# Kernel tuning notes

Hardware: AMD Instinct MI355X
Metric: run time of the kernel (lower is better)

The kernel has to match this reference:

```python
import jax, jax.numpy as jnp
import numpy as np

D, NH, NL, NP, NLAYERS, DFF = 256, 8, 4, 4, 6, 1024
DH = D // NH
SHAPES = [(96, 96), (48, 48), (24, 24), (12, 12)]
STARTS = np.concatenate([[0], np.cumsum([h * w for h, w in SHAPES])[:-1]]).tolist()
LQ = sum(h * w for h, w in SHAPES)
B = 2


def setup_inputs():
    ks = iter(jax.random.split(jax.random.key(0), 64))
    inp = {}
    for i, (h, w) in enumerate(SHAPES):
        inp[f"src{i}"] = jax.random.normal(next(ks), (B, D, h, w), jnp.float32)
        inp[f"pos{i}"] = jax.random.normal(next(ks), (B, D, h, w), jnp.float32) * 0.1
    inp["level_embed"] = jax.random.normal(next(ks), (NL, D), jnp.float32) * 0.02
    W = lambda s, sc: jax.random.normal(next(ks), s, jnp.float32) * sc
    inp["W_off"] = W((NLAYERS, D, NH * NL * NP * 2), 0.01)
    inp["b_off"] = W((NLAYERS, NH * NL * NP * 2), 0.5)
    inp["W_attn"] = W((NLAYERS, D, NH * NL * NP), 0.02)
    inp["b_attn"] = W((NLAYERS, NH * NL * NP), 0.02)
    inp["W_val"] = W((NLAYERS, D, D), 0.05)
    inp["b_val"] = jnp.zeros((NLAYERS, D), jnp.float32)
    inp["W_out"] = W((NLAYERS, D, D), 0.05)
    inp["b_out"] = jnp.zeros((NLAYERS, D), jnp.float32)
    inp["ln1_g"] = jnp.ones((NLAYERS, D), jnp.float32)
    inp["ln1_b"] = jnp.zeros((NLAYERS, D), jnp.float32)
    inp["W_ffn1"] = W((NLAYERS, D, DFF), 0.05)
    inp["b_ffn1"] = jnp.zeros((NLAYERS, DFF), jnp.float32)
    inp["W_ffn2"] = W((NLAYERS, DFF, D), 0.05)
    inp["b_ffn2"] = jnp.zeros((NLAYERS, D), jnp.float32)
    inp["ln2_g"] = jnp.ones((NLAYERS, D), jnp.float32)
    inp["ln2_b"] = jnp.zeros((NLAYERS, D), jnp.float32)
    return inp


def layer_norm(x, g, b):
    mu = x.mean(-1, keepdims=True)
    var = ((x - mu) ** 2).mean(-1, keepdims=True)
    return (x - mu) * jax.lax.rsqrt(var + 1e-5) * g + b


def reference_points():
    refs = []
    for h, w in SHAPES:
        ys = (jnp.arange(h, dtype=jnp.float32) + 0.5) / h
        xs = (jnp.arange(w, dtype=jnp.float32) + 0.5) / w
        gy, gx = jnp.meshgrid(ys, xs, indexing="ij")
        refs.append(jnp.stack([gx.reshape(-1), gy.reshape(-1)], -1))
    return jnp.concatenate(refs, 0)  # [LQ, 2] (x, y); valid_ratios==1 so level-independent


def bilinear(v, loc, H_, W_):
    # v: [B, H*W, NH, DH]; loc: [B, LQ, NH, NP, 2] normalized to [0,1]
    # matches F.grid_sample(mode='bilinear', padding_mode='zeros', align_corners=False)
    x = loc[..., 0] * W_ - 0.5
    y = loc[..., 1] * H_ - 0.5
    x0f, y0f = jnp.floor(x), jnp.floor(y)
    lx, ly = x - x0f, y - y0f
    x0, y0 = x0f.astype(jnp.int32), y0f.astype(jnp.int32)

    def g(xi, yi):
        valid = ((xi >= 0) & (xi < W_) & (yi >= 0) & (yi < H_)).astype(v.dtype)
        flat = jnp.clip(yi, 0, H_ - 1) * W_ + jnp.clip(xi, 0, W_ - 1)  # [B,LQ,NH,NP]
        idx = flat.transpose(0, 1, 3, 2).reshape(B, LQ * NP, NH)
        got = jnp.take_along_axis(v, jnp.broadcast_to(idx[..., None], (B, LQ * NP, NH, DH)), axis=1)
        got = got.reshape(B, LQ, NP, NH, DH).transpose(0, 1, 3, 2, 4)  # [B,LQ,NH,NP,DH]
        return got * valid[..., None]

    return (g(x0, y0) * ((1 - lx) * (1 - ly))[..., None]
            + g(x0 + 1, y0) * (lx * (1 - ly))[..., None]
            + g(x0, y0 + 1) * ((1 - lx) * ly)[..., None]
            + g(x0 + 1, y0 + 1) * (lx * ly)[..., None])


def reference(src0, src1, src2, src3, pos0, pos1, pos2, pos3, level_embed,
              W_off, b_off, W_attn, b_attn, W_val, b_val, W_out, b_out,
              ln1_g, ln1_b, W_ffn1, b_ffn1, W_ffn2, b_ffn2, ln2_g, ln2_b):
    srcs = [src0, src1, src2, src3]
    poss = [pos0, pos1, pos2, pos3]
    x = jnp.concatenate([s.reshape(B, D, -1).transpose(0, 2, 1) for s in srcs], 1)  # [B,LQ,D]
    pos = jnp.concatenate(
        [p.reshape(B, D, -1).transpose(0, 2, 1) + level_embed[i][None, None] for i, p in enumerate(poss)], 1)
    ref = reference_points()  # [LQ,2]
    norm = jnp.array([[w, h] for h, w in SHAPES], jnp.float32)  # [NL,2] = (W,H)

    for li in range(NLAYERS):
        q = x + pos
        off = (q @ W_off[li] + b_off[li]).reshape(B, LQ, NH, NL, NP, 2)
        attn = jax.nn.softmax((q @ W_attn[li] + b_attn[li]).reshape(B, LQ, NH, NL * NP), -1)
        attn = attn.reshape(B, LQ, NH, NL, NP)
        val = (x @ W_val[li] + b_val[li]).reshape(B, LQ, NH, DH)
        loc = ref[None, :, None, None, None, :] + off / norm[None, None, None, :, None, :]
        out = jnp.zeros((B, LQ, NH, DH), x.dtype)
        for l, (h, w) in enumerate(SHAPES):
            vl = val[:, STARTS[l]:STARTS[l] + h * w]
            sampled = bilinear(vl, loc[:, :, :, l], h, w)  # [B,LQ,NH,NP,DH]
            out = out + (sampled * attn[:, :, :, l, :, None]).sum(3)
        out = out.reshape(B, LQ, D) @ W_out[li] + b_out[li]
        x = layer_norm(x + out, ln1_g[li], ln1_b[li])
        ffn = jax.nn.relu(x @ W_ffn1[li] + b_ffn1[li]) @ W_ffn2[li] + b_ffn2[li]
        x = layer_norm(x + ffn, ln2_g[li], ln2_b[li])
    return x
```

## Files before the change

### kernel.cpp

```cpp
#include <hip/hip_runtime.h>
#include <stdint.h>

#define NHEAD  8
#define NLAYER 6
#define BATCH  2
#define LQ     12240
#define MTOK   (BATCH*LQ)
#define MPAD   24576

typedef __attribute__((ext_vector_type(8))) short bf16x8;
typedef __attribute__((ext_vector_type(4))) float f32x4;
typedef __attribute__((ext_vector_type(4))) short s16x4;

__device__ __forceinline__ unsigned short f2bf(float f) {
  union { float f; uint32_t u; } v; v.f = f;
  uint32_t u = v.u;
  uint32_t r = (u + 0x7fffu + ((u >> 16) & 1u)) >> 16;
  return (unsigned short)r;
}
__device__ __forceinline__ float bf2f(unsigned short s) {
  union { uint32_t u; float f; } v; v.u = ((uint32_t)s) << 16;
  return v.f;
}
__device__ __forceinline__ float hi_bf(uint32_t u) {
  union { uint32_t u; float f; } v; v.u = u & 0xffff0000u; return v.f;
}
__device__ __forceinline__ float lo_bf(uint32_t u) {
  union { uint32_t u; float f; } v; v.u = u << 16; return v.f;
}

template<int EPI, int BM>
__global__ __launch_bounds__(256)
void gemm_kernel(const unsigned short* __restrict__ A,
                 const unsigned short* __restrict__ BT,
                 const float* __restrict__ bias,
                 float* __restrict__ Cf,
                 unsigned short* __restrict__ Cb,
                 int K, int ldc)
{
  constexpr int MT = BM / 32;
  __shared__ unsigned short lA[BM*64];
  __shared__ unsigned short lB[128*64];
  const int tid  = threadIdx.x;
  const int lane = tid & 63;
  const int wm = ((tid >> 6) >> 1) * (BM/2);
  const int wn = ((tid >> 6) & 1) * 64;
  const size_t row0 = (size_t)blockIdx.x * BM;
  const size_t col0 = (size_t)blockIdx.y * 128;

  f32x4 acc[MT][4] = {};

  for (int kt = 0; kt < K; kt += 64) {
#pragma unroll
    for (int i = 0; i < MT; ++i) {
      const int slot = i*256 + tid;
      const int r  = slot >> 3;
      const int cs = (slot & 7) ^ (r & 7);
      const unsigned short* ga = A + (row0 + r) * (size_t)K + kt + cs*8;
      __builtin_amdgcn_global_load_lds(
          (const __attribute__((address_space(1))) uint32_t*)ga,
          (__attribute__((address_space(3))) uint32_t*)(&lA[slot*8]), 16, 0, 0);
    }
#pragma unroll
    for (int i = 0; i < 4; ++i) {
      const int slot = i*256 + tid;
      const int r  = slot >> 3;
      const int cs = (slot & 7) ^ (r & 7);
      const unsigned short* gb = BT + (col0 + r) * (size_t)K + kt + cs*8;
      __builtin_amdgcn_global_load_lds(
          (const __attribute__((address_space(1))) uint32_t*)gb,
          (__attribute__((address_space(3))) uint32_t*)(&lB[slot*8]), 16, 0, 0);
    }
    __syncthreads();
#pragma unroll
    for (int kk = 0; kk < 2; ++kk) {
      bf16x8 af[MT], bfv[4];
#pragma unroll
      for (int m = 0; m < MT; ++m) {
        const int r  = wm + m*16 + (lane & 15);
        const int ch = (kk*4 + (lane >> 4)) ^ (r & 7);
        af[m] = *(const bf16x8*)(&lA[r*64 + ch*8]);
      }
#pragma unroll
      for (int n = 0; n < 4; ++n) {
        const int r  = wn + n*16 + (lane & 15);
        const int ch = (kk*4 + (lane >> 4)) ^ (r & 7);
        bfv[n] = *(const bf16x8*)(&lB[r*64 + ch*8]);
      }
#pragma unroll
      for (int m = 0; m < MT; ++m)
#pragma unroll
        for (int n = 0; n < 4; ++n)
          acc[m][n] = __builtin_amdgcn_mfma_f32_16x16x32_bf16(af[m], bfv[n], acc[m][n], 0, 0, 0);
    }
    __syncthreads();
  }

  const int lq = lane >> 4;
  const int lr = lane & 15;
#pragma unroll
  for (int n = 0; n < 4; ++n) {
    const int col = (int)col0 + wn + n*16 + lr;
    const float bv = bias ? bias[col] : 0.f;
#pragma unroll
    for (int m = 0; m < MT; ++m) {
      const size_t rb = row0 + wm + m*16 + lq*4;
#pragma unroll
      for (int i = 0; i < 4; ++i) {
        float v = acc[m][n][i] + bv;
        if (EPI == 2) v = fmaxf(v, 0.f);
        if (EPI == 0) Cf[(rb + i) * (size_t)ldc + col] = v;
        else          Cb[(rb + i) * (size_t)ldc + col] = f2bf(v);
      }
    }
  }
}

template<int MODE>
__global__ __launch_bounds__(256)
void gemm_ln_kernel(const unsigned short* __restrict__ A,
                    const unsigned short* __restrict__ BT,
                    const float* __restrict__ bias,
                    const float* __restrict__ xres,
                    const float* __restrict__ g,
                    const float* __restrict__ bn,
                    const float* __restrict__ posf,
                    float* __restrict__ xoutf,
                    unsigned short* __restrict__ xbf,
                    unsigned short* __restrict__ qbf,
                    float* __restrict__ dout,
                    int K)
{
  __shared__ unsigned short lA[32*64];
  __shared__ unsigned short lB[256*64];
  __shared__ float rs1[4][32];
  __shared__ float rs2[4][32];
  const int tid  = threadIdx.x;
  const int lane = tid & 63;
  const int w    = tid >> 6;
  const size_t row0 = (size_t)blockIdx.x * 32;

  f32x4 acc[2][4] = {};

  for (int kt = 0; kt < K; kt += 64) {
    {
      const int slot = tid;
      const int r  = slot >> 3;
      const int cs = (slot & 7) ^ (r & 7);
      const unsigned short* ga = A + (row0 + r) * (size_t)K + kt + cs*8;
      __builtin_amdgcn_global_load_lds(
          (const __attribute__((address_space(1))) uint32_t*)ga,
          (__attribute__((address_space(3))) uint32_t*)(&lA[slot*8]), 16, 0, 0);
    }
#pragma unroll
    for (int i = 0; i < 8; ++i) {
      const int slot = i*256 + tid;
      const int r  = slot >> 3;
      const int cs = (slot & 7) ^ (r & 7);
      const unsigned short* gb = BT + (size_t)r * K + kt + cs*8;
      __builtin_amdgcn_global_load_lds(
          (const __attribute__((address_space(1))) uint32_t*)gb,
          (__attribute__((address_space(3))) uint32_t*)(&lB[slot*8]), 16, 0, 0);
    }
    __syncthreads();
#pragma unroll
    for (int kk = 0; kk < 2; ++kk) {
      bf16x8 af[2], bfv[4];
#pragma unroll
      for (int m = 0; m < 2; ++m) {
        const int r  = m*16 + (lane & 15);
        const int ch = (kk*4 + (lane >> 4)) ^ (r & 7);
        af[m] = *(const bf16x8*)(&lA[r*64 + ch*8]);
      }
#pragma unroll
      for (int n = 0; n < 4; ++n) {
        const int r  = w*64 + n*16 + (lane & 15);
        const int ch = (kk*4 + (lane >> 4)) ^ (r & 7);
        bfv[n] = *(const bf16x8*)(&lB[r*64 + ch*8]);
      }
#pragma unroll
      for (int m = 0; m < 2; ++m)
#pragma unroll
        for (int n = 0; n < 4; ++n)
          acc[m][n] = __builtin_amdgcn_mfma_f32_16x16x32_bf16(af[m], bfv[n], acc[m][n], 0, 0, 0);
    }
    __syncthreads();
  }

  const int lq = lane >> 4;
  const int lr = lane & 15;
  float bcol[4], gcol[4], bncol[4];
#pragma unroll
  for (int n = 0; n < 4; ++n) {
    const int c = w*64 + n*16 + lr;
    bcol[n]  = bias[c];
    gcol[n]  = g[c];
    bncol[n] = bn[c];
  }
#pragma unroll
  for (int m = 0; m < 2; ++m)
#pragma unroll
    for (int i = 0; i < 4; ++i) {
      const size_t row = row0 + m*16 + lq*4 + i;
#pragma unroll
      for (int n = 0; n < 4; ++n)
        acc[m][n][i] += bcol[n] + xres[row*256 + w*64 + n*16 + lr];
    }
#pragma unroll
  for (int m = 0; m < 2; ++m)
#pragma unroll
    for (int i = 0; i < 4; ++i) {
      float t1 = acc[m][0][i] + acc[m][1][i] + acc[m][2][i] + acc[m][3][i];
      float t2 = acc[m][0][i]*acc[m][0][i] + acc[m][1][i]*acc[m][1][i]
               + acc[m][2][i]*acc[m][2][i] + acc[m][3][i]*acc[m][3][i];
#pragma unroll
      for (int o = 1; o < 16; o <<= 1) {
        t1 += __shfl_xor(t1, o, 64);
        t2 += __shfl_xor(t2, o, 64);
      }
      if (lr == 0) {
        rs1[w][m*16 + lq*4 + i] = t1;
        rs2[w][m*16 + lq*4 + i] = t2;
      }
    }
  __syncthreads();
#pragma unroll
  for (int m = 0; m < 2; ++m)
#pragma unroll
    for (int i = 0; i < 4; ++i) {
      const int r = m*16 + lq*4 + i;
      const float s1 = rs1[0][r] + rs1[1][r] + rs1[2][r] + rs1[3][r];
      const float s2 = rs2[0][r] + rs2[1][r] + rs2[2][r] + rs2[3][r];
      const float mu  = s1 * (1.f/256.f);
      const float var = s2 * (1.f/256.f) - mu*mu;
      const float rstd = rsqrtf(var + 1e-5f);
      const size_t row = row0 + r;
#pragma unroll
      for (int n = 0; n < 4; ++n) {
        const int c = w*64 + n*16 + lr;
        const float nv = (acc[m][n][i] - mu) * rstd * gcol[n] + bncol[n];
        const size_t idx = row*256 + c;
        if (MODE == 2) {
          if (row < MTOK) dout[idx] = nv;
        } else {
          xoutf[idx] = nv;
          xbf[idx]   = f2bf(nv);
          if (MODE == 1) qbf[idx] = f2bf(nv + posf[idx]);
        }
      }
    }
}

__global__ void pack_kernel(const float* __restrict__ s0, const float* __restrict__ s1,
                            const float* __restrict__ s2, const float* __restrict__ s3,
                            const float* __restrict__ p0, const float* __restrict__ p1,
                            const float* __restrict__ p2, const float* __restrict__ p3,
                            const float* __restrict__ lev,
                            float* __restrict__ xo, float* __restrict__ po)
{
  const int bt = blockIdx.x;
  int lvl, st;
  if      (bt < 288) { lvl = 0; st = bt; }
  else if (bt < 360) { lvl = 1; st = bt - 288; }
  else if (bt < 378) { lvl = 2; st = bt - 360; }
  else               { lvl = 3; st = bt - 378; }
  const int HWs[4] = {9216, 2304, 576, 144};
  const int LSs[4] = {0, 9216, 11520, 12096};
  const int hw = HWs[lvl], ls = LSs[lvl];
  const int b = blockIdx.z & 1, isp = blockIdx.z >> 1;
  const float* ins[8] = {s0, s1, s2, s3, p0, p1, p2, p3};
  const float* in = ins[isp*4 + lvl];
  const int sbase = st*32, d0 = blockIdx.y*32;
  __shared__ float tile[32][33];
  const int tx = threadIdx.x, ty = threadIdx.y;
#pragma unroll
  for (int j = 0; j < 4; ++j) {
    int ss = sbase + tx;
    int dd = d0 + ty + j*8;
    tile[ty + j*8][tx] = (ss < hw) ? in[((size_t)b*256 + dd)*hw + ss] : 0.f;
  }
  __syncthreads();
  const float addv = isp ? lev[lvl*256 + d0 + tx] : 0.f;
  float* outp = isp ? po : xo;
#pragma unroll
  for (int j = 0; j < 4; ++j) {
    int ss = sbase + ty + j*8;
    if (ss < hw)
      outp[(size_t)(b*LQ + ls + ss)*256 + d0 + tx] = tile[tx][ty + j*8] + addv;
  }
}

__global__ void wtrans_kernel(const float* __restrict__ Woff, const float* __restrict__ Watt,
                              const float* __restrict__ Wval, const float* __restrict__ Wout,
                              const float* __restrict__ Wf1,  const float* __restrict__ Wf2,
                              unsigned short* __restrict__ WoaT, unsigned short* __restrict__ WvalT,
                              unsigned short* __restrict__ WoutT, unsigned short* __restrict__ Wf1T,
                              unsigned short* __restrict__ Wf2T)
{
  const int li = blockIdx.z;
  const int bt = blockIdx.x;
  const float* in; unsigned short* out; int Kd, Nd, tn, tIdx;
  if      (bt < 64)  { in = Woff + (size_t)li*65536;  out = WoaT  + (size_t)li*98304;         Kd=256;  Nd=256;  tn=8;  tIdx=bt; }
  else if (bt < 96)  { in = Watt + (size_t)li*32768;  out = WoaT  + (size_t)li*98304 + 65536; Kd=256;  Nd=128;  tn=4;  tIdx=bt-64; }
  else if (bt < 160) { in = Wval + (size_t)li*65536;  out = WvalT + (size_t)li*65536;         Kd=256;  Nd=256;  tn=8;  tIdx=bt-96; }
  else if (bt < 224) { in = Wout + (size_t)li*65536;  out = WoutT + (size_t)li*65536;         Kd=256;  Nd=256;  tn=8;  tIdx=bt-160; }
  else if (bt < 480) { in = Wf1  + (size_t)li*262144; out = Wf1T  + (size_t)li*262144;        Kd=256;  Nd=1024; tn=32; tIdx=bt-224; }
  else               { in = Wf2  + (size_t)li*262144; out = Wf2T  + (size_t)li*262144;        Kd=1024; Nd=256;  tn=8;  tIdx=bt-480; }
  const int kt = tIdx / tn, nt = tIdx - kt*tn;
  const int k0 = kt*32, n0 = nt*32;
  __shared__ float tile[32][33];
  const int tx = threadIdx.x, ty = threadIdx.y;
#pragma unroll
  for (int j = 0; j < 4; ++j)
    tile[ty + j*8][tx] = in[(size_t)(k0 + ty + j*8) * Nd + n0 + tx];
  __syncthreads();
#pragma unroll
  for (int j = 0; j < 4; ++j)
    out[(size_t)(n0 + ty + j*8) * Kd + k0 + tx] = f2bf(tile[tx][ty + j*8]);
}

__global__ void bias_concat_kernel(const float* __restrict__ boff, const float* __restrict__ batt,
                                   float* __restrict__ boa)
{
  const int li = blockIdx.x, i = threadIdx.x;
  boa[li*384 + i] = (i < 256) ? boff[li*256 + i] : batt[li*128 + (i - 256)];
}

__global__ void prep_kernel(const float* __restrict__ x, const float* __restrict__ pos,
                            unsigned short* __restrict__ xbf, unsigned short* __restrict__ qbf)
{
  const int idx = blockIdx.x * 256 + threadIdx.x;
  const int row = idx >> 6;
  s16x4 xb = {}, qb = {};
  if (row < MTOK) {
    const f32x4 xv = *(const f32x4*)(x + (size_t)idx*4);
    const f32x4 pv = *(const f32x4*)(pos + (size_t)idx*4);
#pragma unroll
    for (int j = 0; j < 4; ++j) {
      xb[j] = (short)f2bf(xv[j]);
      qb[j] = (short)f2bf(xv[j] + pv[j]);
    }
  }
  *(s16x4*)(xbf + (size_t)idx*4) = xb;
  *(s16x4*)(qbf + (size_t)idx*4) = qb;
}

__global__ __launch_bounds__(256)
void sample_kernel(const float* __restrict__ Coa, const unsigned short* __restrict__ val,
                   unsigned short* __restrict__ outbf)
{
  __shared__ int4  pdo[32][17];
  __shared__ f32x4 pdw[32][17];
  const int tid = threadIdx.x;
  const int gi  = tid >> 3;
  const int g   = blockIdx.x * 32 + gi;
  const int t   = g >> 3, h = g & 7;
  const int b   = (t >= LQ) ? 1 : 0;

  {
    const int i0 = tid & 7;
    int4  ov0 = {0,0,0,0}, ov1 = {0,0,0,0};
    f32x4 wv0 = {0,0,0,0}, wv1 = {0,0,0,0};
    if (t < MTOK) {
      const int q = t - b * LQ;
      float refx, refy;
      if      (q < 9216)  { const int r = q;         const int rw = r/96; refx = (r - rw*96 + 0.5f)*(1.f/96.f); refy = (rw + 0.5f)*(1.f/96.f); }
      else if (q < 11520) { const int r = q - 9216;  const int rw = r/48; refx = (r - rw*48 + 0.5f)*(1.f/48.f); refy = (rw + 0.5f)*(1.f/48.f); }
      else if (q < 12096) { const int r = q - 11520; const int rw = r/24; refx = (r - rw*24 + 0.5f)*(1.f/24.f); refy = (rw + 0.5f)*(1.f/24.f); }
      else                { const int r = q - 12096; const int rw = r/12; refx = (r - rw*12 + 0.5f)*(1.f/12.f); refy = (rw + 0.5f)*(1.f/12.f); }
      const size_t crow = (size_t)t * 384;
      const float l0 = Coa[crow + 256 + h*16 + i0];
      const float l1 = Coa[crow + 256 + h*16 + i0 + 8];
      float mx = fmaxf(l0, l1);
#pragma unroll
      for (int m = 1; m < 8; m <<= 1) mx = fmaxf(mx, __shfl_xor(mx, m, 64));
      const float e0 = __expf(l0 - mx), e1 = __expf(l1 - mx);
      float sum = e0 + e1;
#pragma unroll
      for (int m = 1; m < 8; m <<= 1) sum += __shfl_xor(sum, m, 64);
      const float inv = 1.f / sum;

      auto mkpd = [&](int i, float aw, int4& ov, f32x4& wv) {
        const int l    = i >> 2;
        const int wl   = (l == 0) ? 96 : (l == 1) ? 48 : (l == 2) ? 24 : 12;
        const int base = (l == 0) ? 0  : (l == 1) ? 9216 : (l == 2) ? 11520 : 12096;
        const float ox = Coa[crow + h*32 + 2*i];
        const float oy = Coa[crow + h*32 + 2*i + 1];
        const float fw = (float)wl;
        const float xx = refx*fw + ox - 0.5f;
        const float yy = refy*fw + oy - 0.5f;
        const float xf = floorf(xx), yf = floorf(yy);
        const int x0 = (int)xf, y0 = (int)yf;
        const float lx = xx - xf, ly = yy - yf;
        const bool vx0 = (x0   >= 0) & (x0   < wl);
        const bool vx1 = (x0+1 >= 0) & (x0+1 < wl);
        const bool vy0 = (y0   >= 0) & (y0   < wl);
        const bool vy1 = (y0+1 >= 0) & (y0+1 < wl);
        const int cx0 = min(max(x0,   0), wl-1);
        const int cx1 = min(max(x0+1, 0), wl-1);
        const int cy0 = min(max(y0,   0), wl-1);
        const int cy1 = min(max(y0+1, 0), wl-1);
        ov.x = (base + cy0*wl + cx0) * 512;
        ov.y = (base + cy0*wl + cx1) * 512;
        ov.z = (base + cy1*wl + cx0) * 512;
        ov.w = (base + cy1*wl + cx1) * 512;
        wv[0] = (vx0 & vy0) ? (1.f-lx)*(1.f-ly)*aw : 0.f;
        wv[1] = (vx1 & vy0) ? lx*(1.f-ly)*aw       : 0.f;
        wv[2] = (vx0 & vy1) ? (1.f-lx)*ly*aw       : 0.f;
        wv[3] = (vx1 & vy1) ? lx*ly*aw             : 0.f;
      };
      mkpd(i0,     e0 * inv, ov0, wv0);
      mkpd(i0 + 8, e1 * inv, ov1, wv1);
    }
    pdo[gi][i0]     = ov0;  pdw[gi][i0]     = wv0;
    pdo[gi][i0 + 8] = ov1;  pdw[gi][i0 + 8] = wv1;
  }
  __syncthreads();

  const int lane8 = tid & 7;
  const char* vb = (const char*)(val + (size_t)b*LQ*256 + h*32 + lane8*4);
  const int4*  po8 = pdo[gi];
  const f32x4* pw8 = pdw[gi];
  f32x4 a0 = {}, a1 = {}, a2 = {}, a3 = {};
#pragma unroll
  for (int p = 0; p < 16; ++p) {
    const int4  o = po8[p];
    const f32x4 w = pw8[p];
    const uint2 c0 = *(const uint2*)(vb + o.x);
    const uint2 c1 = *(const uint2*)(vb + o.y);
    const uint2 c2 = *(const uint2*)(vb + o.z);
    const uint2 c3 = *(const uint2*)(vb + o.w);
    a0[0] += w[0]*lo_bf(c0.x); a0[1] += w[0]*hi_bf(c0.x); a0[2] += w[0]*lo_bf(c0.y); a0[3] += w[0]*hi_bf(c0.y);
    a1[0] += w[1]*lo_bf(c1.x); a1[1] += w[1]*hi_bf(c1.x); a1[2] += w[1]*lo_bf(c1.y); a1[3] += w[1]*hi_bf(c1.y);
    a2[0] += w[2]*lo_bf(c2.x); a2[1] += w[2]*hi_bf(c2.x); a2[2] += w[2]*lo_bf(c2.y); a2[3] += w[2]*hi_bf(c2.y);
    a3[0] += w[3]*lo_bf(c3.x); a3[1] += w[3]*hi_bf(c3.x); a3[2] += w[3]*lo_bf(c3.y); a3[3] += w[3]*hi_bf(c3.y);
  }
  s16x4 ob;
#pragma unroll
  for (int j = 0; j < 4; ++j) ob[j] = (short)f2bf((a0[j] + a1[j]) + (a2[j] + a3[j]));
  *(s16x4*)(outbf + (size_t)t*256 + h*32 + lane8*4) = ob;
}

extern "C" void kernel_launch(void* const* d_in, const int* in_sizes, int n_in,
                              void* d_out, int out_size, void* d_ws, size_t ws_size,
                              hipStream_t stream)
{
  const float* src0 = (const float*)d_in[0];
  const float* pos0 = (const float*)d_in[1];
  const float* src1 = (const float*)d_in[2];
  const float* pos1 = (const float*)d_in[3];
  const float* src2 = (const float*)d_in[4];
  const float* pos2 = (const float*)d_in[5];
  const float* src3 = (const float*)d_in[6];
  const float* pos3 = (const float*)d_in[7];
  const float* lev  = (const float*)d_in[8];
  const float* W_off= (const float*)d_in[9];
  const float* b_off= (const float*)d_in[10];
  const float* W_att= (const float*)d_in[11];
  const float* b_att= (const float*)d_in[12];
  const float* W_val= (const float*)d_in[13];
  const float* b_val= (const float*)d_in[14];
  const float* W_out= (const float*)d_in[15];
  const float* b_out= (const float*)d_in[16];
  const float* ln1g = (const float*)d_in[17];
  const float* ln1b = (const float*)d_in[18];
  const float* W_f1 = (const float*)d_in[19];
  const float* b_f1 = (const float*)d_in[20];
  const float* W_f2 = (const float*)d_in[21];
  const float* b_f2 = (const float*)d_in[22];
  const float* ln2g = (const float*)d_in[23];
  const float* ln2b = (const float*)d_in[24];

  char* wp = (char*)d_ws;
  auto take = [&](size_t bytes) { char* p = wp; wp += (bytes + 255) & ~(size_t)255; return p; };
  float* x    = (float*)take((size_t)MPAD*256*4);
  float* pos  = (float*)take((size_t)MPAD*256*4);
  float* Coa  = (float*)take((size_t)MPAD*384*4);
  unsigned short* xbf    = (unsigned short*)take((size_t)MPAD*256*2);
  unsigned short* qbf    = (unsigned short*)take((size_t)MPAD*256*2);
  unsigned short* valbf  = (unsigned short*)take((size_t)MPAD*256*2);
  unsigned short* sampbf = (unsigned short*)take((size_t)MPAD*256*2);
  unsigned short* h1bf   = (unsigned short*)take((size_t)MPAD*1024*2);
  unsigned short* WoaT   = (unsigned short*)take((size_t)NLAYER*384*256*2);
  unsigned short* WvalT  = (unsigned short*)take((size_t)NLAYER*256*256*2);
  unsigned short* WoutT  = (unsigned short*)take((size_t)NLAYER*256*256*2);
  unsigned short* Wf1T   = (unsigned short*)take((size_t)NLAYER*1024*256*2);
  unsigned short* Wf2T   = (unsigned short*)take((size_t)NLAYER*256*1024*2);
  float* boa  = (float*)take((size_t)NLAYER*384*4);

  dim3 tb(32, 8);
  pack_kernel<<<dim3(383, 8, 4), tb, 0, stream>>>(src0, src1, src2, src3,
                                                  pos0, pos1, pos2, pos3, lev, x, pos);
  wtrans_kernel<<<dim3(736, 1, 6), tb, 0, stream>>>(W_off, W_att, W_val, W_out, W_f1, W_f2,
                                                    WoaT, WvalT, WoutT, Wf1T, Wf2T);
  bias_concat_kernel<<<NLAYER, 384, 0, stream>>>(b_off, b_att, boa);
  prep_kernel<<<MPAD/4, 256, 0, stream>>>(x, pos, xbf, qbf);

  for (int li = 0; li < NLAYER; ++li) {
    gemm_kernel<0,64><<<dim3(MPAD/64, 3), 256, 0, stream>>>(qbf, WoaT + (size_t)li*98304,
        boa + li*384, Coa, nullptr, 256, 384);
    gemm_kernel<1,64><<<dim3(MPAD/64, 2), 256, 0, stream>>>(xbf, WvalT + (size_t)li*65536,
        b_val + li*256, nullptr, valbf, 256, 256);
    sample_kernel<<<MPAD/4, 256, 0, stream>>>(Coa, valbf, sampbf);
    gemm_ln_kernel<0><<<MPAD/32, 256, 0, stream>>>(sampbf, WoutT + (size_t)li*65536,
        b_out + li*256, x, ln1g + li*256, ln1b + li*256, nullptr,
        x, xbf, nullptr, nullptr, 256);
    gemm_kernel<2,128><<<dim3(MPAD/128, 8), 256, 0, stream>>>(xbf, Wf1T + (size_t)li*262144,
        b_f1 + li*1024, nullptr, h1bf, 256, 1024);
    if (li < NLAYER-1)
      gemm_ln_kernel<1><<<MPAD/32, 256, 0, stream>>>(h1bf, Wf2T + (size_t)li*262144,
          b_f2 + li*256, x, ln2g + li*256, ln2b + li*256, pos,
          x, xbf, qbf, nullptr, 1024);
    else
      gemm_ln_kernel<2><<<MPAD/32, 256, 0, stream>>>(h1bf, Wf2T + (size_t)li*262144,
          b_f2 + li*256, x, ln2g + li*256, ln2b + li*256, nullptr,
          nullptr, nullptr, nullptr, (float*)d_out, 1024);
  }
}
```

Measured before the change: 996.2 us.

## Store value head-major and gather adjacent bilinear corners with one contiguous load

```diff
diff --git a/kernel.cpp b/kernel.cpp
--- a/kernel.cpp
+++ b/kernel.cpp
@@ -109,8 +109,19 @@
       for (int i = 0; i < 4; ++i) {
         float v = acc[m][n][i] + bv;
         if (EPI == 2) v = fmaxf(v, 0.f);
-        if (EPI == 0) Cf[(rb + i) * (size_t)ldc + col] = v;
-        else          Cb[(rb + i) * (size_t)ldc + col] = f2bf(v);
+        if (EPI == 3) {
+          const size_t row = rb + i;
+          if (row < MTOK) {
+            const int bb = (row >= LQ) ? 1 : 0;
+            const int q  = (int)row - bb * LQ;
+            const int hh = col >> 5, ch = col & 31;
+            Cb[((size_t)(bb*8 + hh) * LQ + q) * 32 + ch] = f2bf(v);
+          }
+        } else if (EPI == 0) {
+          Cf[(rb + i) * (size_t)ldc + col] = v;
+        } else {
+          Cb[(rb + i) * (size_t)ldc + col] = f2bf(v);
+        }
       }
     }
   }
@@ -346,21 +357,21 @@
 }
 
 __global__ __launch_bounds__(256)
-void sample_kernel(const float* __restrict__ Coa, const unsigned short* __restrict__ val,
+void sample_kernel(const float* __restrict__ Coa, const unsigned short* __restrict__ valh,
                    unsigned short* __restrict__ outbf)
 {
-  __shared__ int4  pdo[32][17];
-  __shared__ f32x4 pdw[32][17];
+  __shared__ int2  pdo[16][16];
+  __shared__ f32x4 pdw[16][16];
   const int tid = threadIdx.x;
-  const int gi  = tid >> 3;
-  const int g   = blockIdx.x * 32 + gi;
+  const int gi  = tid >> 4;
+  const int g   = blockIdx.x * 16 + gi;
   const int t   = g >> 3, h = g & 7;
   const int b   = (t >= LQ) ? 1 : 0;
 
   {
-    const int i0 = tid & 7;
-    int4  ov0 = {0,0,0,0}, ov1 = {0,0,0,0};
-    f32x4 wv0 = {0,0,0,0}, wv1 = {0,0,0,0};
+    const int i = tid & 15;
+    int2  ov = {0, 0};
+    f32x4 wv = {0.f, 0.f, 0.f, 0.f};
     if (t < MTOK) {
       const int q = t - b * LQ;
       float refx, refy;
@@ -369,76 +380,77 @@
       else if (q < 12096) { const int r = q - 11520; const int rw = r/24; refx = (r - rw*24 + 0.5f)*(1.f/24.f); refy = (rw + 0.5f)*(1.f/24.f); }
       else                { const int r = q - 12096; const int rw = r/12; refx = (r - rw*12 + 0.5f)*(1.f/12.f); refy = (rw + 0.5f)*(1.f/12.f); }
       const size_t crow = (size_t)t * 384;
-      const float l0 = Coa[crow + 256 + h*16 + i0];
-      const float l1 = Coa[crow + 256 + h*16 + i0 + 8];
-      float mx = fmaxf(l0, l1);
-#pragma unroll
-      for (int m = 1; m < 8; m <<= 1) mx = fmaxf(mx, __shfl_xor(mx, m, 64));
-      const float e0 = __expf(l0 - mx), e1 = __expf(l1 - mx);
-      float sum = e0 + e1;
-#pragma unroll
-      for (int m = 1; m < 8; m <<= 1) sum += __shfl_xor(sum, m, 64);
-      const float inv = 1.f / sum;
-
-      auto mkpd = [&](int i, float aw, int4& ov, f32x4& wv) {
-        const int l    = i >> 2;
-        const int wl   = (l == 0) ? 96 : (l == 1) ? 48 : (l == 2) ? 24 : 12;
-        const int base = (l == 0) ? 0  : (l == 1) ? 9216 : (l == 2) ? 11520 : 12096;
-        const float ox = Coa[crow + h*32 + 2*i];
-        const float oy = Coa[crow + h*32 + 2*i + 1];
-        const float fw = (float)wl;
-        const float xx = refx*fw + ox - 0.5f;
-        const float yy = refy*fw + oy - 0.5f;
-        const float xf = floorf(xx), yf = floorf(yy);
-        const int x0 = (int)xf, y0 = (int)yf;
-        const float lx = xx - xf, ly = yy - yf;
-        const bool vx0 = (x0   >= 0) & (x0   < wl);
-        const bool vx1 = (x0+1 >= 0) & (x0+1 < wl);
-        const bool vy0 = (y0   >= 0) & (y0   < wl);
-        const bool vy1 = (y0+1 >= 0) & (y0+1 < wl);
-        const int cx0 = min(max(x0,   0), wl-1);
-        const int cx1 = min(max(x0+1, 0), wl-1);
-        const int cy0 = min(max(y0,   0), wl-1);
-        const int cy1 = min(max(y0+1, 0), wl-1);
-        ov.x = (base + cy0*wl + cx0) * 512;
-        ov.y = (base + cy0*wl + cx1) * 512;
-        ov.z = (base + cy1*wl + cx0) * 512;
-        ov.w = (base + cy1*wl + cx1) * 512;
-        wv[0] = (vx0 & vy0) ? (1.f-lx)*(1.f-ly)*aw : 0.f;
-        wv[1] = (vx1 & vy0) ? lx*(1.f-ly)*aw       : 0.f;
-        wv[2] = (vx0 & vy1) ? (1.f-lx)*ly*aw       : 0.f;
-        wv[3] = (vx1 & vy1) ? lx*ly*aw             : 0.f;
-      };
-      mkpd(i0,     e0 * inv, ov0, wv0);
-      mkpd(i0 + 8, e1 * inv, ov1, wv1);
-    }
-    pdo[gi][i0]     = ov0;  pdw[gi][i0]     = wv0;
-    pdo[gi][i0 + 8] = ov1;  pdw[gi][i0 + 8] = wv1;
+      const float logit = Coa[crow + 256 + h*16 + i];
+      float mx = logit;
+#pragma unroll
+      for (int m = 1; m < 16; m <<= 1) mx = fmaxf(mx, __shfl_xor(mx, m, 64));
+      const float e = __expf(logit - mx);
+      float sum = e;
+#pragma unroll
+      for (int m = 1; m < 16; m <<= 1) sum += __shfl_xor(sum, m, 64);
+      const float aw = e / sum;
+
+      const int l    = i >> 2;
+      const int wl   = (l == 0) ? 96 : (l == 1) ? 48 : (l == 2) ? 24 : 12;
+      const int base = (l == 0) ? 0  : (l == 1) ? 9216 : (l == 2) ? 11520 : 12096;
+      const float2 oxy = *(const float2*)(&Coa[crow + h*32 + 2*i]);
+      const float fw = (float)wl;
+      const float xx = refx*fw + oxy.x - 0.5f;
+      const float yy = refy*fw + oxy.y - 0.5f;
+      const float xf = floorf(xx), yf = floorf(yy);
+      const int x0 = (int)xf, y0 = (int)yf;
+      const float lx = xx - xf, ly = yy - yf;
+      const bool vx0 = (x0   >= 0) & (x0   < wl);
+      const bool vx1 = (x0+1 >= 0) & (x0+1 < wl);
+      const bool vy0 = (y0   >= 0) & (y0   < wl);
+      const bool vy1 = (y0+1 >= 0) & (y0+1 < wl);
+      const int cy0 = min(max(y0,   0), wl-1);
+      const int cy1 = min(max(y0+1, 0), wl-1);
+      const int hb = (b*8 + h) * LQ;
+      int eT = hb + base + cy0*wl + x0;
+      int eB = hb + base + cy1*wl + x0;
+      eT = max(eT, 0);
+      eB = max(eB, 0);
+      ov.x = eT * 64;
+      ov.y = eB * 64;
+      wv[0] = (vx0 & vy0) ? (1.f-lx)*(1.f-ly)*aw : 0.f;
+      wv[1] = (vx0 & vy1) ? (1.f-lx)*ly*aw       : 0.f;
+      wv[2] = (vx1 & vy0) ? lx*(1.f-ly)*aw       : 0.f;
+      wv[3] = (vx1 & vy1) ? lx*ly*aw             : 0.f;
+    }
+    pdo[gi][i] = ov;
+    pdw[gi][i] = wv;
   }
   __syncthreads();
 
-  const int lane8 = tid & 7;
-  const char* vb = (const char*)(val + (size_t)b*LQ*256 + h*32 + lane8*4);
-  const int4*  po8 = pdo[gi];
-  const f32x4* pw8 = pdw[gi];
-  f32x4 a0 = {}, a1 = {}, a2 = {}, a3 = {};
+  const int laneByte = (tid & 15) * 8;
+  const int halfOff  = tid & 8;
+  const char* vb = (const char*)valh;
+  const int2* po = pdo[gi];
+  f32x4 aT = {}, aB = {};
 #pragma unroll
   for (int p = 0; p < 16; ++p) {
-    const int4  o = po8[p];
-    const f32x4 w = pw8[p];
-    const uint2 c0 = *(const uint2*)(vb + o.x);
-    const uint2 c1 = *(const uint2*)(vb + o.y);
-    const uint2 c2 = *(const uint2*)(vb + o.z);
-    const uint2 c3 = *(const uint2*)(vb + o.w);
-    a0[0] += w[0]*lo_bf(c0.x); a0[1] += w[0]*hi_bf(c0.x); a0[2] += w[0]*lo_bf(c0.y); a0[3] += w[0]*hi_bf(c0.y);
-    a1[0] += w[1]*lo_bf(c1.x); a1[1] += w[1]*hi_bf(c1.x); a1[2] += w[1]*lo_bf(c1.y); a1[3] += w[1]*hi_bf(c1.y);
-    a2[0] += w[2]*lo_bf(c2.x); a2[1] += w[2]*hi_bf(c2.x); a2[2] += w[2]*lo_bf(c2.y); a2[3] += w[2]*hi_bf(c2.y);
-    a3[0] += w[3]*lo_bf(c3.x); a3[1] += w[3]*hi_bf(c3.x); a3[2] += w[3]*lo_bf(c3.y); a3[3] += w[3]*hi_bf(c3.y);
-  }
-  s16x4 ob;
-#pragma unroll
-  for (int j = 0; j < 4; ++j) ob[j] = (short)f2bf((a0[j] + a1[j]) + (a2[j] + a3[j]));
-  *(s16x4*)(outbf + (size_t)t*256 + h*32 + lane8*4) = ob;
+    const int2   o = po[p];
+    const float2 w = *(const float2*)((const char*)&pdw[gi][p] + halfOff);
+    const uint2 cT = *(const uint2*)(vb + (uint32_t)(o.x + laneByte));
+    const uint2 cB = *(const uint2*)(vb + (uint32_t)(o.y + laneByte));
+    aT[0] += w.x*lo_bf(cT.x); aT[1] += w.x*hi_bf(cT.x);
+    aT[2] += w.x*lo_bf(cT.y); aT[3] += w.x*hi_bf(cT.y);
+    aB[0] += w.y*lo_bf(cB.x); aB[1] += w.y*hi_bf(cB.x);
+    aB[2] += w.y*lo_bf(cB.y); aB[3] += w.y*hi_bf(cB.y);
+  }
+  f32x4 s;
+#pragma unroll
+  for (int j = 0; j < 4; ++j) {
+    s[j] = aT[j] + aB[j];
+    s[j] += __shfl_xor(s[j], 8, 64);
+  }
+  if ((tid & 8) == 0) {
+    s16x4 ob;
+#pragma unroll
+    for (int j = 0; j < 4; ++j) ob[j] = (short)f2bf(s[j]);
+    *(s16x4*)(outbf + (size_t)t*256 + h*32 + (tid & 7)*4) = ob;
+  }
 }
 
 extern "C" void kernel_launch(void* const* d_in, const int* in_sizes, int n_in,
@@ -478,7 +490,7 @@
   float* Coa  = (float*)take((size_t)MPAD*384*4);
   unsigned short* xbf    = (unsigned short*)take((size_t)MPAD*256*2);
   unsigned short* qbf    = (unsigned short*)take((size_t)MPAD*256*2);
-  unsigned short* valbf  = (unsigned short*)take((size_t)MPAD*256*2);
+  unsigned short* valh   = (unsigned short*)take((size_t)16*LQ*32*2 + 256);
   unsigned short* sampbf = (unsigned short*)take((size_t)MPAD*256*2);
   unsigned short* h1bf   = (unsigned short*)take((size_t)MPAD*1024*2);
   unsigned short* WoaT   = (unsigned short*)take((size_t)NLAYER*384*256*2);
@@ -499,9 +511,9 @@
   for (int li = 0; li < NLAYER; ++li) {
     gemm_kernel<0,64><<<dim3(MPAD/64, 3), 256, 0, stream>>>(qbf, WoaT + (size_t)li*98304,
         boa + li*384, Coa, nullptr, 256, 384);
-    gemm_kernel<1,64><<<dim3(MPAD/64, 2), 256, 0, stream>>>(xbf, WvalT + (size_t)li*65536,
-        b_val + li*256, nullptr, valbf, 256, 256);
-    sample_kernel<<<MPAD/4, 256, 0, stream>>>(Coa, valbf, sampbf);
+    gemm_kernel<3,64><<<dim3(MPAD/64, 2), 256, 0, stream>>>(xbf, WvalT + (size_t)li*65536,
+        b_val + li*256, nullptr, valh, 256, 256);
+    sample_kernel<<<MPAD/2, 256, 0, stream>>>(Coa, valh, sampbf);
     gemm_ln_kernel<0><<<MPAD/32, 256, 0, stream>>>(sampbf, WoutT + (size_t)li*65536,
         b_out + li*256, x, ln1g + li*256, ln1b + li*256, nullptr,
         x, xbf, nullptr, nullptr, 256);
```

Measured after the change: 1.057 ms. 1.06x slower.
